# Performance work log

Measured on AMD Instinct MI355X. Metric: run time of the kernel, lower is better.

Reference implementation:

```python
import jax, jax.numpy as jnp
import numpy as np

B, S, H = 2, 1024, 1024
E, I, K = 8, 3584, 2


def setup_inputs() -> dict:
    key = jax.random.key(0)
    k1, k2, k3, k4, k5 = jax.random.split(key, 5)
    scale_h = 1.0 / np.sqrt(H)
    scale_i = 1.0 / np.sqrt(I)
    return {
        "hidden_states": jax.random.normal(k1, (B, S, H), dtype=jnp.float32),
        "gate_w": jax.random.normal(k2, (E, H), dtype=jnp.float32) * scale_h,
        "w1": jax.random.normal(k3, (E, I, H), dtype=jnp.float32) * scale_h,
        "w2": jax.random.normal(k4, (E, H, I), dtype=jnp.float32) * scale_i,
        "w3": jax.random.normal(k5, (E, I, H), dtype=jnp.float32) * scale_h,
    }


def reference(hidden_states, gate_w, w1, w2, w3):
    b, s, h = hidden_states.shape
    x = hidden_states.reshape(-1, h)  # [T, H]
    # router: logits -> float32 softmax -> top-k -> renormalize
    router_logits = x @ gate_w.T  # [T, E]
    probs = jax.nn.softmax(router_logits.astype(jnp.float32), axis=-1)
    topw, topi = jax.lax.top_k(probs, K)  # [T, K]
    topw = topw / jnp.sum(topw, axis=-1, keepdims=True)
    topw = topw.astype(x.dtype)
    # per-token per-expert gate weight (0 for unselected experts) -> dense
    # combine is mathematically identical to gather/scatter dispatch
    gate = jnp.sum(jax.nn.one_hot(topi, E, dtype=x.dtype) * topw[..., None], axis=1)  # [T, E]
    # grouped SwiGLU FFN over all experts
    h1 = jnp.einsum('th,eih->tei', x, w1)
    h3 = jnp.einsum('th,eih->tei', x, w3)
    g = jax.nn.silu(h1) * h3  # [T, E, I]
    y = jnp.einsum('tei,ehi->teh', g, w2)  # [T, E, H]
    out = jnp.einsum('te,teh->th', gate, y)
    return out.reshape(b, s, h)
```

## Files before the change

kernel.cpp:

```cpp
#include <hip/hip_runtime.h>
#include <stdint.h>

#define T_TOK 2048
#define HDIM 1024
#define NEXP 8
#define IDIM 3584
#define MAXTILE 40

#define WS_CNT   0
#define WS_BASE  64
#define WS_TE    128
#define WS_TM    384
#define WS_NT    640
#define WS_TOK   704
#define WS_GW    (WS_TOK + NEXP * T_TOK * 4)
#define WS_XB    (WS_GW + NEXP * T_TOK * 4)
#define WS_G     (WS_XB + T_TOK * HDIM * 2)

typedef __attribute__((ext_vector_type(8))) short bf16x8;
typedef __attribute__((ext_vector_type(16))) float f32x16;

__device__ __forceinline__ unsigned short f2bf(float f) {
    union { float f; unsigned int u; } a; a.f = f;
    unsigned int u = a.u;
    return (unsigned short)((u + 0x7fffu + ((u >> 16) & 1u)) >> 16);
}

__device__ __forceinline__ unsigned int cvt_pk_bf16(float lo, float hi) {
    unsigned int r;
    asm("v_cvt_pk_bf16_f32 %0, %1, %2" : "=v"(r) : "v"(lo), "v"(hi));
    return r;
}

__device__ __forceinline__ uint4 pack8(const float4 a, const float4 b) {
    uint4 r;
    r.x = cvt_pk_bf16(a.x, a.y);
    r.y = cvt_pk_bf16(a.z, a.w);
    r.z = cvt_pk_bf16(b.x, b.y);
    r.w = cvt_pk_bf16(b.z, b.w);
    return r;
}

__device__ __forceinline__ void gload16(const void* gsrc, void* ldst) {
    __builtin_amdgcn_global_load_lds(
        (const __attribute__((address_space(1))) unsigned int*)gsrc,
        (__attribute__((address_space(3))) unsigned int*)ldst, 16, 0, 0);
}

__global__ __launch_bounds__(256) void xcvt_kernel(
    const float* __restrict__ x, unsigned short* __restrict__ xb)
{
    int i = (blockIdx.x * 256 + threadIdx.x) * 8;
    float4 a = *(const float4*)(x + i);
    float4 b = *(const float4*)(x + i + 4);
    *(uint4*)(xb + i) = pack8(a, b);
}

__global__ __launch_bounds__(256) void router_kernel(
    const float* __restrict__ x, const float* __restrict__ gate_w,
    int* __restrict__ cnt, int* __restrict__ tok, float* __restrict__ gw)
{
    int t = blockIdx.x * 4 + (threadIdx.x >> 6);
    int lane = threadIdx.x & 63;
    if (t >= T_TOK) return;
    const float* xr = x + (size_t)t * HDIM;
    float part[NEXP];
#pragma unroll
    for (int e = 0; e < NEXP; e++) part[e] = 0.f;
    for (int h = lane; h < HDIM; h += 64) {
        float xv = xr[h];
#pragma unroll
        for (int e = 0; e < NEXP; e++) part[e] += xv * gate_w[e * HDIM + h];
    }
#pragma unroll
    for (int e = 0; e < NEXP; e++) {
        float v = part[e];
#pragma unroll
        for (int o = 32; o > 0; o >>= 1) v += __shfl_xor(v, o);
        part[e] = v;
    }
    if (lane == 0) {
        int i0 = 0; float v0 = part[0];
#pragma unroll
        for (int e = 1; e < NEXP; e++) if (part[e] > v0) { v0 = part[e]; i0 = e; }
        int i1 = -1; float v1 = -3.4e38f;
#pragma unroll
        for (int e = 0; e < NEXP; e++) if (e != i0 && part[e] > v1) { v1 = part[e]; i1 = e; }
        float d = __expf(v1 - v0);
        float w1v = d / (1.f + d);
        float w0v = 1.f - w1v;
        int p0 = atomicAdd(&cnt[i0], 1);
        tok[i0 * T_TOK + p0] = t; gw[i0 * T_TOK + p0] = w0v;
        int p1 = atomicAdd(&cnt[i1], 1);
        tok[i1 * T_TOK + p1] = t; gw[i1 * T_TOK + p1] = w1v;
    }
}

__global__ void scan_kernel(const int* __restrict__ cnt, int* __restrict__ base,
                            int* __restrict__ tileE, int* __restrict__ tileM,
                            int* __restrict__ ntot)
{
    if (threadIdx.x == 0) {
        int s = 0, nt = 0;
        for (int e = 0; e < NEXP; e++) {
            base[e] = s; s += cnt[e];
            for (int m0 = 0; m0 < cnt[e]; m0 += 128) {
                tileE[nt] = e; tileM[nt] = m0; nt++;
            }
        }
        *ntot = nt;
    }
}

__global__ __launch_bounds__(256, 3) void ffn1_mfma(
    const unsigned short* __restrict__ xb,
    const float* __restrict__ w1,
    const float* __restrict__ w3,
    const int* __restrict__ cnt, const int* __restrict__ base,
    const int* __restrict__ tok,
    const int* __restrict__ tileE, const int* __restrict__ tileM,
    const int* __restrict__ ntot,
    unsigned short* __restrict__ g)
{
    const int ti = blockIdx.y;
    if (ti >= *ntot) return;
    const int e = tileE[ti];
    const int m0 = tileM[ti];
    const int cntE = cnt[e];
    const int i0 = blockIdx.x * 64;
    const int tid = threadIdx.x;
    const int lane = tid & 63;
    const int wid = tid >> 6;

    __shared__ __align__(16) unsigned char lds[49152];

    const int xrr = (lane >> 3);
    const unsigned xoff = ((((unsigned)(lane & 7)) * 16) ^ (((unsigned)xrr) << 4)) >> 1;
    const unsigned short* xsrc[4];
#pragma unroll
    for (int i = 0; i < 4; i++) {
        int row = wid * 32 + i * 8 + xrr;
        int t = tok[e * T_TOK + min(m0 + row, cntE - 1)];
        xsrc[i] = xb + (size_t)t * HDIM + xoff;
    }

    const int rw = tid >> 2;
    const int kq = tid & 3;
    const unsigned swzW = ((unsigned)(rw & 7)) << 4;
    const unsigned wd0 = (((unsigned)kq) * 32) ^ swzW;
    const unsigned wd1 = (((unsigned)kq) * 32 + 16) ^ swzW;
    const float* w1e = w1 + ((size_t)e * IDIM + i0 + rw) * HDIM + kq * 16;
    const float* w3e = w3 + ((size_t)e * IDIM + i0 + rw) * HDIM + kq * 16;

    f32x16 acc1[2], acc3[2];
#pragma unroll
    for (int a = 0; a < 2; a++)
#pragma unroll
        for (int r = 0; r < 16; r++) { acc1[a][r] = 0.f; acc3[a][r] = 0.f; }

    const int wr = wid >> 1;
    const int wc = wid & 1;
    const unsigned lrow = (unsigned)(lane & 31);
    const unsigned lswz = (lrow & 7) << 4;
    const unsigned hi16 = (unsigned)((lane >> 5) * 16);
    const unsigned aRow = (wr * 64 + lrow) * 128;
    const unsigned bRow1 = 32768u + (wc * 32 + lrow) * 128;
    const unsigned bRow3 = 40960u + (wc * 32 + lrow) * 128;

    float4 wva[4], wvb[4];

#pragma unroll
    for (int i = 0; i < 4; i++)
        gload16(xsrc[i], lds + (wid * 32 + i * 8) * 128);
#pragma unroll
    for (int i = 0; i < 4; i++) {
        wva[i] = *(const float4*)(w1e + i * 4);
        wvb[i] = *(const float4*)(w3e + i * 4);
    }

    for (int st = 0; st < HDIM / 64; st++) {
        const unsigned xsb = (unsigned)(st & 1) * 16384u;
        const int k0 = st * 64;
        __syncthreads();
        *(uint4*)(lds + 32768u + rw * 128 + wd0) = pack8(wva[0], wva[1]);
        *(uint4*)(lds + 32768u + rw * 128 + wd1) = pack8(wva[2], wva[3]);
        *(uint4*)(lds + 40960u + rw * 128 + wd0) = pack8(wvb[0], wvb[1]);
        *(uint4*)(lds + 40960u + rw * 128 + wd1) = pack8(wvb[2], wvb[3]);
        __syncthreads();

        if (k0 + 64 < HDIM) {
            const unsigned xnb = xsb ^ 16384u;
#pragma unroll
            for (int i = 0; i < 4; i++)
                gload16(xsrc[i] + k0 + 64, lds + xnb + (wid * 32 + i * 8) * 128);
#pragma unroll
            for (int i = 0; i < 4; i++) {
                wva[i] = *(const float4*)(w1e + k0 + 64 + i * 4);
                wvb[i] = *(const float4*)(w3e + k0 + 64 + i * 4);
            }
        }

#pragma unroll
        for (int s = 0; s < 4; s++) {
            const unsigned off = (((unsigned)(s * 32)) + hi16) ^ lswz;
            bf16x8 a0 = *(const bf16x8*)(lds + xsb + aRow + off);
            bf16x8 a1 = *(const bf16x8*)(lds + xsb + aRow + 32 * 128 + off);
            bf16x8 b1 = *(const bf16x8*)(lds + bRow1 + off);
            bf16x8 b3 = *(const bf16x8*)(lds + bRow3 + off);
            acc1[0] = __builtin_amdgcn_mfma_f32_32x32x16_bf16(a0, b1, acc1[0], 0, 0, 0);
            acc1[1] = __builtin_amdgcn_mfma_f32_32x32x16_bf16(a1, b1, acc1[1], 0, 0, 0);
            acc3[0] = __builtin_amdgcn_mfma_f32_32x32x16_bf16(a0, b3, acc3[0], 0, 0, 0);
            acc3[1] = __builtin_amdgcn_mfma_f32_32x32x16_bf16(a1, b3, acc3[1], 0, 0, 0);
        }
    }

    const int pbase = base[e] + m0;
    const int colI = i0 + wc * 32 + (int)lrow;
    const int rb4 = 4 * (lane >> 5);
#pragma unroll
    for (int ma = 0; ma < 2; ma++) {
#pragma unroll
        for (int r = 0; r < 16; r++) {
            int row = (r & 3) + 8 * (r >> 2) + rb4;
            int m = wr * 64 + ma * 32 + row;
            if (m0 + m < cntE) {
                float h1 = acc1[ma][r], h3 = acc3[ma][r];
                float v = (h1 / (1.f + __expf(-h1))) * h3;
                g[(size_t)(pbase + m) * IDIM + colI] = f2bf(v);
            }
        }
    }
}

__global__ __launch_bounds__(256, 4) void ffn2_mfma(
    const unsigned short* __restrict__ g,
    const float* __restrict__ w2,
    const int* __restrict__ cnt, const int* __restrict__ base,
    const int* __restrict__ tok, const float* __restrict__ gw,
    const int* __restrict__ tileE, const int* __restrict__ tileM,
    const int* __restrict__ ntot,
    float* __restrict__ out)
{
    const int ti = blockIdx.y;
    if (ti >= *ntot) return;
    const int e = tileE[ti];
    const int m0 = tileM[ti];
    const int cntE = cnt[e];
    const int pane = blockIdx.x;
    const int h0 = (pane & 15) * 64;
    const int ks = pane >> 4;
    const int tid = threadIdx.x;
    const int lane = tid & 63;
    const int wid = tid >> 6;

    __shared__ __align__(16) unsigned char lds[40960];

    const int kbeg = ks * (IDIM / 4);

    const int xrr = (lane >> 3);
    const unsigned xoff = ((((unsigned)(lane & 7)) * 16) ^ (((unsigned)xrr) << 4)) >> 1;
    const unsigned short* gsrc[4];
    const int be = base[e];
#pragma unroll
    for (int i = 0; i < 4; i++) {
        int row = wid * 32 + i * 8 + xrr;
        int grow = be + min(m0 + row, cntE - 1);
        gsrc[i] = g + (size_t)grow * IDIM + kbeg + xoff;
    }

    const int rw = tid >> 2;
    const int kq = tid & 3;
    const unsigned swzW = ((unsigned)(rw & 7)) << 4;
    const unsigned wd0 = (((unsigned)kq) * 32) ^ swzW;
    const unsigned wd1 = (((unsigned)kq) * 32 + 16) ^ swzW;
    const float* w2e = w2 + ((size_t)e * HDIM + h0 + rw) * IDIM + kbeg + kq * 16;

    f32x16 acc[2];
#pragma unroll
    for (int a = 0; a < 2; a++)
#pragma unroll
        for (int r = 0; r < 16; r++) acc[a][r] = 0.f;

    const int wr = wid >> 1;
    const int wc = wid & 1;
    const unsigned lrow = (unsigned)(lane & 31);
    const unsigned lswz = (lrow & 7) << 4;
    const unsigned hi16 = (unsigned)((lane >> 5) * 16);
    const unsigned aRow = (wr * 64 + lrow) * 128;
    const unsigned bRow = 32768u + (wc * 32 + lrow) * 128;

    float4 wv[4];
#pragma unroll
    for (int i = 0; i < 4; i++)
        gload16(gsrc[i], lds + (wid * 32 + i * 8) * 128);
#pragma unroll
    for (int i = 0; i < 4; i++)
        wv[i] = *(const float4*)(w2e + i * 4);

    const int NST = (IDIM / 4) / 64;
    for (int st = 0; st < NST; st++) {
        const unsigned xsb = (unsigned)(st & 1) * 16384u;
        const int k0 = st * 64;
        __syncthreads();
        *(uint4*)(lds + 32768u + rw * 128 + wd0) = pack8(wv[0], wv[1]);
        *(uint4*)(lds + 32768u + rw * 128 + wd1) = pack8(wv[2], wv[3]);
        __syncthreads();

        if (st + 1 < NST) {
            const unsigned xnb = xsb ^ 16384u;
#pragma unroll
            for (int i = 0; i < 4; i++)
                gload16(gsrc[i] + k0 + 64, lds + xnb + (wid * 32 + i * 8) * 128);
#pragma unroll
            for (int i = 0; i < 4; i++)
                wv[i] = *(const float4*)(w2e + k0 + 64 + i * 4);
        }

#pragma unroll
        for (int s = 0; s < 4; s++) {
            const unsigned off = (((unsigned)(s * 32)) + hi16) ^ lswz;
            bf16x8 a0 = *(const bf16x8*)(lds + xsb + aRow + off);
            bf16x8 a1 = *(const bf16x8*)(lds + xsb + aRow + 32 * 128 + off);
            bf16x8 b0 = *(const bf16x8*)(lds + bRow + off);
            acc[0] = __builtin_amdgcn_mfma_f32_32x32x16_bf16(a0, b0, acc[0], 0, 0, 0);
            acc[1] = __builtin_amdgcn_mfma_f32_32x32x16_bf16(a1, b0, acc[1], 0, 0, 0);
        }
    }

    const int rb4 = 4 * (lane >> 5);
    const int hcol = h0 + wc * 32 + (int)lrow;
#pragma unroll
    for (int ma = 0; ma < 2; ma++) {
#pragma unroll
        for (int r = 0; r < 16; r++) {
            int row = (r & 3) + 8 * (r >> 2) + rb4;
            int m = wr * 64 + ma * 32 + row;
            if (m0 + m < cntE) {
                int idx = e * T_TOK + m0 + m;
                int t = tok[idx];
                float wgt = gw[idx];
                atomicAdd(out + (size_t)t * HDIM + hcol, wgt * acc[ma][r]);
            }
        }
    }
}

extern "C" void kernel_launch(void* const* d_in, const int* in_sizes, int n_in,
                              void* d_out, int out_size, void* d_ws, size_t ws_size,
                              hipStream_t stream) {
    const float* x      = (const float*)d_in[0];
    const float* gate_w = (const float*)d_in[1];
    const float* w1     = (const float*)d_in[2];
    const float* w2     = (const float*)d_in[3];
    const float* w3     = (const float*)d_in[4];
    float* out = (float*)d_out;
    char* ws = (char*)d_ws;
    int* cnt   = (int*)(ws + WS_CNT);
    int* base  = (int*)(ws + WS_BASE);
    int* tileE = (int*)(ws + WS_TE);
    int* tileM = (int*)(ws + WS_TM);
    int* ntot  = (int*)(ws + WS_NT);
    int* tok   = (int*)(ws + WS_TOK);
    float* gw  = (float*)(ws + WS_GW);
    unsigned short* xb = (unsigned short*)(ws + WS_XB);
    unsigned short* g  = (unsigned short*)(ws + WS_G);

    hipMemsetAsync(cnt, 0, 64, stream);
    hipMemsetAsync(d_out, 0, (size_t)out_size * sizeof(float), stream);

    xcvt_kernel<<<T_TOK * HDIM / (256 * 8), 256, 0, stream>>>(x, xb);
    router_kernel<<<T_TOK / 4, 256, 0, stream>>>(x, gate_w, cnt, tok, gw);
    scan_kernel<<<1, 64, 0, stream>>>(cnt, base, tileE, tileM, ntot);
    ffn1_mfma<<<dim3(IDIM / 64, MAXTILE), 256, 0, stream>>>(xb, w1, w3, cnt, base, tok, tileE, tileM, ntot, g);
    ffn2_mfma<<<dim3(64, MAXTILE), 256, 0, stream>>>(g, w2, cnt, base, tok, gw, tileE, tileM, ntot, out);
}
```

Before: 333.9 us.

## Double-buffer weight tiles in LDS and use a single barrier per k-step

Both FFN kernels now double-buffer the packed bf16 weight tile in LDS alongside the activation tile. Weight registers are prefetched two steps ahead, with explicit vmcnt waits and sched barriers, so each k-iteration needs only one barrier instead of two. The goal is to overlap global weight loads and bf16 packing with MFMA work and to cut synchronisation stalls. In exchange LDS use grows, which lowers the occupancy bounds (ffn1 from 3 to 2 blocks, ffn2 from 4 to 3). The hand-written waitcnt counts must match the exact number of outstanding loads.

```diff
diff --git a/kernel.cpp b/kernel.cpp
--- a/kernel.cpp
+++ b/kernel.cpp
@@ -46,6 +46,8 @@
         (const __attribute__((address_space(1))) unsigned int*)gsrc,
         (__attribute__((address_space(3))) unsigned int*)ldst, 16, 0, 0);
 }
+
+#define SB() __builtin_amdgcn_sched_barrier(0)
 
 __global__ __launch_bounds__(256) void xcvt_kernel(
     const float* __restrict__ x, unsigned short* __restrict__ xb)
@@ -112,7 +114,7 @@
     }
 }
 
-__global__ __launch_bounds__(256, 3) void ffn1_mfma(
+__global__ __launch_bounds__(256, 2) void ffn1_mfma(
     const unsigned short* __restrict__ xb,
     const float* __restrict__ w1,
     const float* __restrict__ w3,
@@ -132,7 +134,7 @@
     const int lane = tid & 63;
     const int wid = tid >> 6;
 
-    __shared__ __align__(16) unsigned char lds[49152];
+    __shared__ __align__(16) unsigned char lds[65536];
 
     const int xrr = (lane >> 3);
     const unsigned xoff = ((((unsigned)(lane & 7)) * 16) ^ (((unsigned)xrr) << 4)) >> 1;
@@ -163,56 +165,71 @@
     const unsigned lrow = (unsigned)(lane & 31);
     const unsigned lswz = (lrow & 7) << 4;
     const unsigned hi16 = (unsigned)((lane >> 5) * 16);
-    const unsigned aRow = (wr * 64 + lrow) * 128;
-    const unsigned bRow1 = 32768u + (wc * 32 + lrow) * 128;
-    const unsigned bRow3 = 40960u + (wc * 32 + lrow) * 128;
+    const unsigned aOff  = (wr * 64 + lrow) * 128;
+    const unsigned b1Off = 16384u + (wc * 32 + lrow) * 128;
+    const unsigned b3Off = 24576u + (wc * 32 + lrow) * 128;
+    const unsigned xdst = (unsigned)(wid * 32) * 128;
 
     float4 wva[4], wvb[4];
 
 #pragma unroll
     for (int i = 0; i < 4; i++)
-        gload16(xsrc[i], lds + (wid * 32 + i * 8) * 128);
+        gload16(xsrc[i], lds + xdst + (unsigned)(i * 8) * 128);
 #pragma unroll
     for (int i = 0; i < 4; i++) {
         wva[i] = *(const float4*)(w1e + i * 4);
         wvb[i] = *(const float4*)(w3e + i * 4);
     }
+    asm volatile("s_waitcnt vmcnt(0)" ::: "memory");
+    *(uint4*)(lds + 16384u + rw * 128 + wd0) = pack8(wva[0], wva[1]);
+    *(uint4*)(lds + 16384u + rw * 128 + wd1) = pack8(wva[2], wva[3]);
+    *(uint4*)(lds + 24576u + rw * 128 + wd0) = pack8(wvb[0], wvb[1]);
+    *(uint4*)(lds + 24576u + rw * 128 + wd1) = pack8(wvb[2], wvb[3]);
+#pragma unroll
+    for (int i = 0; i < 4; i++) {
+        wva[i] = *(const float4*)(w1e + 64 + i * 4);
+        wvb[i] = *(const float4*)(w3e + 64 + i * 4);
+    }
+    __syncthreads();
 
     for (int st = 0; st < HDIM / 64; st++) {
-        const unsigned xsb = (unsigned)(st & 1) * 16384u;
-        const int k0 = st * 64;
-        __syncthreads();
-        *(uint4*)(lds + 32768u + rw * 128 + wd0) = pack8(wva[0], wva[1]);
-        *(uint4*)(lds + 32768u + rw * 128 + wd1) = pack8(wva[2], wva[3]);
-        *(uint4*)(lds + 40960u + rw * 128 + wd0) = pack8(wvb[0], wvb[1]);
-        *(uint4*)(lds + 40960u + rw * 128 + wd1) = pack8(wvb[2], wvb[3]);
-        __syncthreads();
-
-        if (k0 + 64 < HDIM) {
-            const unsigned xnb = xsb ^ 16384u;
-#pragma unroll
-            for (int i = 0; i < 4; i++)
-                gload16(xsrc[i] + k0 + 64, lds + xnb + (wid * 32 + i * 8) * 128);
-#pragma unroll
-            for (int i = 0; i < 4; i++) {
-                wva[i] = *(const float4*)(w1e + k0 + 64 + i * 4);
-                wvb[i] = *(const float4*)(w3e + k0 + 64 + i * 4);
-            }
-        }
-
+        const unsigned cb = (unsigned)(st & 1) * 32768u;
+        const unsigned nb = cb ^ 32768u;
+        SB();
+        const int kg = min((st + 1) * 64, HDIM - 64);
+#pragma unroll
+        for (int i = 0; i < 4; i++)
+            gload16(xsrc[i] + kg, lds + nb + xdst + (unsigned)(i * 8) * 128);
+        SB();
+        *(uint4*)(lds + nb + 16384u + rw * 128 + wd0) = pack8(wva[0], wva[1]);
+        *(uint4*)(lds + nb + 16384u + rw * 128 + wd1) = pack8(wva[2], wva[3]);
+        *(uint4*)(lds + nb + 24576u + rw * 128 + wd0) = pack8(wvb[0], wvb[1]);
+        *(uint4*)(lds + nb + 24576u + rw * 128 + wd1) = pack8(wvb[2], wvb[3]);
+        SB();
+        const int kw = min((st + 2) * 64, HDIM - 64);
+#pragma unroll
+        for (int i = 0; i < 4; i++) {
+            wva[i] = *(const float4*)(w1e + kw + i * 4);
+            wvb[i] = *(const float4*)(w3e + kw + i * 4);
+        }
+        SB();
 #pragma unroll
         for (int s = 0; s < 4; s++) {
             const unsigned off = (((unsigned)(s * 32)) + hi16) ^ lswz;
-            bf16x8 a0 = *(const bf16x8*)(lds + xsb + aRow + off);
-            bf16x8 a1 = *(const bf16x8*)(lds + xsb + aRow + 32 * 128 + off);
-            bf16x8 b1 = *(const bf16x8*)(lds + bRow1 + off);
-            bf16x8 b3 = *(const bf16x8*)(lds + bRow3 + off);
-            acc1[0] = __builtin_amdgcn_mfma_f32_32x32x16_bf16(a0, b1, acc1[0], 0, 0, 0);
-            acc1[1] = __builtin_amdgcn_mfma_f32_32x32x16_bf16(a1, b1, acc1[1], 0, 0, 0);
-            acc3[0] = __builtin_amdgcn_mfma_f32_32x32x16_bf16(a0, b3, acc3[0], 0, 0, 0);
-            acc3[1] = __builtin_amdgcn_mfma_f32_32x32x16_bf16(a1, b3, acc3[1], 0, 0, 0);
-        }
-    }
+            bf16x8 a0 = *(const bf16x8*)(lds + cb + aOff + off);
+            bf16x8 a1 = *(const bf16x8*)(lds + cb + aOff + 32 * 128 + off);
+            bf16x8 p0 = *(const bf16x8*)(lds + cb + b1Off + off);
+            bf16x8 q0 = *(const bf16x8*)(lds + cb + b3Off + off);
+            acc1[0] = __builtin_amdgcn_mfma_f32_32x32x16_bf16(a0, p0, acc1[0], 0, 0, 0);
+            acc1[1] = __builtin_amdgcn_mfma_f32_32x32x16_bf16(a1, p0, acc1[1], 0, 0, 0);
+            acc3[0] = __builtin_amdgcn_mfma_f32_32x32x16_bf16(a0, q0, acc3[0], 0, 0, 0);
+            acc3[1] = __builtin_amdgcn_mfma_f32_32x32x16_bf16(a1, q0, acc3[1], 0, 0, 0);
+        }
+        asm volatile("s_waitcnt vmcnt(8) lgkmcnt(0)" ::: "memory");
+        SB();
+        __builtin_amdgcn_s_barrier();
+    }
+    asm volatile("s_waitcnt vmcnt(0)" ::: "memory");
 
     const int pbase = base[e] + m0;
     const int colI = i0 + wc * 32 + (int)lrow;
@@ -232,7 +249,7 @@
     }
 }
 
-__global__ __launch_bounds__(256, 4) void ffn2_mfma(
+__global__ __launch_bounds__(256, 3) void ffn2_mfma(
     const unsigned short* __restrict__ g,
     const float* __restrict__ w2,
     const int* __restrict__ cnt, const int* __restrict__ base,
@@ -253,9 +270,10 @@
     const int lane = tid & 63;
     const int wid = tid >> 6;
 
-    __shared__ __align__(16) unsigned char lds[40960];
+    __shared__ __align__(16) unsigned char lds[49152];
 
     const int kbeg = ks * (IDIM / 4);
+    const int KSP = IDIM / 4;
 
     const int xrr = (lane >> 3);
     const unsigned xoff = ((((unsigned)(lane & 7)) * 16) ^ (((unsigned)xrr) << 4)) >> 1;
@@ -286,46 +304,58 @@
     const unsigned lrow = (unsigned)(lane & 31);
     const unsigned lswz = (lrow & 7) << 4;
     const unsigned hi16 = (unsigned)((lane >> 5) * 16);
-    const unsigned aRow = (wr * 64 + lrow) * 128;
-    const unsigned bRow = 32768u + (wc * 32 + lrow) * 128;
+    const unsigned aOff = (wr * 64 + lrow) * 128;
+    const unsigned bOff = 16384u + (wc * 32 + lrow) * 128;
+    const unsigned xdst = (unsigned)(wid * 32) * 128;
 
     float4 wv[4];
+
 #pragma unroll
     for (int i = 0; i < 4; i++)
-        gload16(gsrc[i], lds + (wid * 32 + i * 8) * 128);
+        gload16(gsrc[i], lds + xdst + (unsigned)(i * 8) * 128);
 #pragma unroll
     for (int i = 0; i < 4; i++)
         wv[i] = *(const float4*)(w2e + i * 4);
-
-    const int NST = (IDIM / 4) / 64;
+    asm volatile("s_waitcnt vmcnt(0)" ::: "memory");
+    *(uint4*)(lds + 16384u + rw * 128 + wd0) = pack8(wv[0], wv[1]);
+    *(uint4*)(lds + 16384u + rw * 128 + wd1) = pack8(wv[2], wv[3]);
+#pragma unroll
+    for (int i = 0; i < 4; i++)
+        wv[i] = *(const float4*)(w2e + 64 + i * 4);
+    __syncthreads();
+
+    const int NST = KSP / 64;
     for (int st = 0; st < NST; st++) {
-        const unsigned xsb = (unsigned)(st & 1) * 16384u;
-        const int k0 = st * 64;
-        __syncthreads();
-        *(uint4*)(lds + 32768u + rw * 128 + wd0) = pack8(wv[0], wv[1]);
-        *(uint4*)(lds + 32768u + rw * 128 + wd1) = pack8(wv[2], wv[3]);
-        __syncthreads();
-
-        if (st + 1 < NST) {
-            const unsigned xnb = xsb ^ 16384u;
-#pragma unroll
-            for (int i = 0; i < 4; i++)
-                gload16(gsrc[i] + k0 + 64, lds + xnb + (wid * 32 + i * 8) * 128);
-#pragma unroll
-            for (int i = 0; i < 4; i++)
-                wv[i] = *(const float4*)(w2e + k0 + 64 + i * 4);
-        }
-
+        const unsigned cb = (unsigned)(st & 1) * 24576u;
+        const unsigned nb = cb ^ 24576u;
+        SB();
+        const int kg = min((st + 1) * 64, KSP - 64);
+#pragma unroll
+        for (int i = 0; i < 4; i++)
+            gload16(gsrc[i] + kg, lds + nb + xdst + (unsigned)(i * 8) * 128);
+        SB();
+        *(uint4*)(lds + nb + 16384u + rw * 128 + wd0) = pack8(wv[0], wv[1]);
+        *(uint4*)(lds + nb + 16384u + rw * 128 + wd1) = pack8(wv[2], wv[3]);
+        SB();
+        const int kw = min((st + 2) * 64, KSP - 64);
+#pragma unroll
+        for (int i = 0; i < 4; i++)
+            wv[i] = *(const float4*)(w2e + kw + i * 4);
+        SB();
 #pragma unroll
         for (int s = 0; s < 4; s++) {
             const unsigned off = (((unsigned)(s * 32)) + hi16) ^ lswz;
-            bf16x8 a0 = *(const bf16x8*)(lds + xsb + aRow + off);
-            bf16x8 a1 = *(const bf16x8*)(lds + xsb + aRow + 32 * 128 + off);
-            bf16x8 b0 = *(const bf16x8*)(lds + bRow + off);
+            bf16x8 a0 = *(const bf16x8*)(lds + cb + aOff + off);
+            bf16x8 a1 = *(const bf16x8*)(lds + cb + aOff + 32 * 128 + off);
+            bf16x8 b0 = *(const bf16x8*)(lds + cb + bOff + off);
             acc[0] = __builtin_amdgcn_mfma_f32_32x32x16_bf16(a0, b0, acc[0], 0, 0, 0);
             acc[1] = __builtin_amdgcn_mfma_f32_32x32x16_bf16(a1, b0, acc[1], 0, 0, 0);
         }
-    }
+        asm volatile("s_waitcnt vmcnt(4) lgkmcnt(0)" ::: "memory");
+        SB();
+        __builtin_amdgcn_s_barrier();
+    }
+    asm volatile("s_waitcnt vmcnt(0)" ::: "memory");
 
     const int rb4 = 4 * (lane >> 5);
     const int hcol = h0 + wc * 32 + (int)lrow;
```

New measurement: 350.0 us. +4.8%, slower.

## Load activation fragments directly to registers and pipeline weight staging with single barrier

Applied to the files above, without the earlier changes.

Both FFN kernels stop staging the token activations through LDS. Each wave now loads its own 32-row A fragments straight from global memory into registers, and only the bf16-converted weight tiles go through LDS, in a small double buffer with a 32-wide K step. The loop is software-pipelined two and three steps ahead and uses one barrier per step instead of two. Each wave now owns 32 rows across all 64 columns instead of a 64x32 quadrant. LDS use drops sharply, which may help occupancy, but A reads are now uncoalesced per-lane 16-byte global loads and there are twice as many barrier steps.

```diff
diff --git a/kernel.cpp b/kernel.cpp
--- a/kernel.cpp
+++ b/kernel.cpp
@@ -41,12 +41,6 @@
     return r;
 }
 
-__device__ __forceinline__ void gload16(const void* gsrc, void* ldst) {
-    __builtin_amdgcn_global_load_lds(
-        (const __attribute__((address_space(1))) unsigned int*)gsrc,
-        (__attribute__((address_space(3))) unsigned int*)ldst, 16, 0, 0);
-}
-
 __global__ __launch_bounds__(256) void xcvt_kernel(
     const float* __restrict__ x, unsigned short* __restrict__ xb)
 {
@@ -111,6 +105,38 @@
         *ntot = nt;
     }
 }
+
+#define F1_MFMA(AF, RO)                                                        \
+    _Pragma("unroll")                                                          \
+    for (int s = 0; s < 2; s++) {                                              \
+      bf16x8 b1a = *(const bf16x8*)(lds + (RO) + bfo[0][s]);                   \
+      bf16x8 b1b = *(const bf16x8*)(lds + (RO) + bfo[1][s]);                   \
+      bf16x8 b3a = *(const bf16x8*)(lds + 8192u + (RO) + bfo[0][s]);           \
+      bf16x8 b3b = *(const bf16x8*)(lds + 8192u + (RO) + bfo[1][s]);           \
+      acc1[0] = __builtin_amdgcn_mfma_f32_32x32x16_bf16(AF[s], b1a, acc1[0], 0, 0, 0); \
+      acc1[1] = __builtin_amdgcn_mfma_f32_32x32x16_bf16(AF[s], b1b, acc1[1], 0, 0, 0); \
+      acc3[0] = __builtin_amdgcn_mfma_f32_32x32x16_bf16(AF[s], b3a, acc3[0], 0, 0, 0); \
+      acc3[1] = __builtin_amdgcn_mfma_f32_32x32x16_bf16(AF[s], b3b, acc3[1], 0, 0, 0); \
+    }
+
+#define F1_STEP(ST, AF, W1C, W3C)                                              \
+  {                                                                            \
+    F1_MFMA(AF, ((unsigned)((ST) & 1)) * 4096u)                                \
+    const unsigned wo = ((unsigned)(((ST) + 1) & 1)) * 4096u;                  \
+    *(uint4*)(lds + wo + wdst) = pack8(W1C[0], W1C[1]);                        \
+    *(uint4*)(lds + 8192u + wo + wdst) = pack8(W3C[0], W3C[1]);                \
+    const int ka = min(((ST) + 2) * 32, HDIM - 32);                            \
+    AF[0] = *(const bf16x8*)(arow + ka);                                       \
+    AF[1] = *(const bf16x8*)(arow + ka + 16);                                  \
+    const int kw = min(((ST) + 3) * 32, HDIM - 32);                            \
+    W1C[0] = *(const float4*)(w1e + kw);                                       \
+    W1C[1] = *(const float4*)(w1e + kw + 4);                                   \
+    W3C[0] = *(const float4*)(w3e + kw);                                       \
+    W3C[1] = *(const float4*)(w3e + kw + 4);                                   \
+    asm volatile("s_waitcnt lgkmcnt(0)" ::: "memory");                         \
+    __builtin_amdgcn_sched_barrier(0);                                         \
+    __builtin_amdgcn_s_barrier();                                              \
+  }
 
 __global__ __launch_bounds__(256, 3) void ffn1_mfma(
     const unsigned short* __restrict__ xb,
@@ -132,25 +158,34 @@
     const int lane = tid & 63;
     const int wid = tid >> 6;
 
-    __shared__ __align__(16) unsigned char lds[49152];
-
-    const int xrr = (lane >> 3);
-    const unsigned xoff = ((((unsigned)(lane & 7)) * 16) ^ (((unsigned)xrr) << 4)) >> 1;
-    const unsigned short* xsrc[4];
-#pragma unroll
-    for (int i = 0; i < 4; i++) {
-        int row = wid * 32 + i * 8 + xrr;
+    __shared__ __align__(16) unsigned char lds[16384];
+
+    const int fr = lane & 31;
+    const int hi = lane >> 5;
+
+    const unsigned short* arow;
+    {
+        int row = wid * 32 + fr;
         int t = tok[e * T_TOK + min(m0 + row, cntE - 1)];
-        xsrc[i] = xb + (size_t)t * HDIM + xoff;
-    }
-
-    const int rw = tid >> 2;
-    const int kq = tid & 3;
-    const unsigned swzW = ((unsigned)(rw & 7)) << 4;
-    const unsigned wd0 = (((unsigned)kq) * 32) ^ swzW;
-    const unsigned wd1 = (((unsigned)kq) * 32 + 16) ^ swzW;
-    const float* w1e = w1 + ((size_t)e * IDIM + i0 + rw) * HDIM + kq * 16;
-    const float* w3e = w3 + ((size_t)e * IDIM + i0 + rw) * HDIM + kq * 16;
+        arow = xb + (size_t)t * HDIM + hi * 8;
+    }
+
+    unsigned bfo[2][2];
+#pragma unroll
+    for (int f2 = 0; f2 < 2; f2++)
+#pragma unroll
+        for (int s = 0; s < 2; s++) {
+            unsigned row = (unsigned)(f2 * 32 + fr);
+            unsigned slot = ((unsigned)(s * 2 + hi)) ^ ((row >> 1) & 3u);
+            bfo[f2][s] = row * 64u + slot * 16u;
+        }
+
+    const int srow = tid >> 2;
+    const int c4 = tid & 3;
+    const unsigned wdst = (unsigned)srow * 64u +
+                          (((unsigned)c4 ^ (((unsigned)srow >> 1) & 3u)) * 16u);
+    const float* w1e = w1 + ((size_t)e * IDIM + i0 + srow) * HDIM + c4 * 8;
+    const float* w3e = w3 + ((size_t)e * IDIM + i0 + srow) * HDIM + c4 * 8;
 
     f32x16 acc1[2], acc3[2];
 #pragma unroll
@@ -158,79 +193,74 @@
 #pragma unroll
         for (int r = 0; r < 16; r++) { acc1[a][r] = 0.f; acc3[a][r] = 0.f; }
 
-    const int wr = wid >> 1;
-    const int wc = wid & 1;
-    const unsigned lrow = (unsigned)(lane & 31);
-    const unsigned lswz = (lrow & 7) << 4;
-    const unsigned hi16 = (unsigned)((lane >> 5) * 16);
-    const unsigned aRow = (wr * 64 + lrow) * 128;
-    const unsigned bRow1 = 32768u + (wc * 32 + lrow) * 128;
-    const unsigned bRow3 = 40960u + (wc * 32 + lrow) * 128;
-
-    float4 wva[4], wvb[4];
-
-#pragma unroll
-    for (int i = 0; i < 4; i++)
-        gload16(xsrc[i], lds + (wid * 32 + i * 8) * 128);
-#pragma unroll
-    for (int i = 0; i < 4; i++) {
-        wva[i] = *(const float4*)(w1e + i * 4);
-        wvb[i] = *(const float4*)(w3e + i * 4);
-    }
-
-    for (int st = 0; st < HDIM / 64; st++) {
-        const unsigned xsb = (unsigned)(st & 1) * 16384u;
-        const int k0 = st * 64;
-        __syncthreads();
-        *(uint4*)(lds + 32768u + rw * 128 + wd0) = pack8(wva[0], wva[1]);
-        *(uint4*)(lds + 32768u + rw * 128 + wd1) = pack8(wva[2], wva[3]);
-        *(uint4*)(lds + 40960u + rw * 128 + wd0) = pack8(wvb[0], wvb[1]);
-        *(uint4*)(lds + 40960u + rw * 128 + wd1) = pack8(wvb[2], wvb[3]);
-        __syncthreads();
-
-        if (k0 + 64 < HDIM) {
-            const unsigned xnb = xsb ^ 16384u;
-#pragma unroll
-            for (int i = 0; i < 4; i++)
-                gload16(xsrc[i] + k0 + 64, lds + xnb + (wid * 32 + i * 8) * 128);
-#pragma unroll
-            for (int i = 0; i < 4; i++) {
-                wva[i] = *(const float4*)(w1e + k0 + 64 + i * 4);
-                wvb[i] = *(const float4*)(w3e + k0 + 64 + i * 4);
-            }
-        }
-
-#pragma unroll
-        for (int s = 0; s < 4; s++) {
-            const unsigned off = (((unsigned)(s * 32)) + hi16) ^ lswz;
-            bf16x8 a0 = *(const bf16x8*)(lds + xsb + aRow + off);
-            bf16x8 a1 = *(const bf16x8*)(lds + xsb + aRow + 32 * 128 + off);
-            bf16x8 b1 = *(const bf16x8*)(lds + bRow1 + off);
-            bf16x8 b3 = *(const bf16x8*)(lds + bRow3 + off);
-            acc1[0] = __builtin_amdgcn_mfma_f32_32x32x16_bf16(a0, b1, acc1[0], 0, 0, 0);
-            acc1[1] = __builtin_amdgcn_mfma_f32_32x32x16_bf16(a1, b1, acc1[1], 0, 0, 0);
-            acc3[0] = __builtin_amdgcn_mfma_f32_32x32x16_bf16(a0, b3, acc3[0], 0, 0, 0);
-            acc3[1] = __builtin_amdgcn_mfma_f32_32x32x16_bf16(a1, b3, acc3[1], 0, 0, 0);
-        }
+    bf16x8 af0[2], af1[2];
+    float4 w1cA[2], w3cA[2], w1cB[2], w3cB[2];
+
+    {
+        float4 t0 = *(const float4*)(w1e);
+        float4 t1 = *(const float4*)(w1e + 4);
+        float4 t2 = *(const float4*)(w3e);
+        float4 t3 = *(const float4*)(w3e + 4);
+        *(uint4*)(lds + wdst) = pack8(t0, t1);
+        *(uint4*)(lds + 8192u + wdst) = pack8(t2, t3);
+    }
+    af0[0] = *(const bf16x8*)(arow);
+    af0[1] = *(const bf16x8*)(arow + 16);
+    af1[0] = *(const bf16x8*)(arow + 32);
+    af1[1] = *(const bf16x8*)(arow + 48);
+    w1cA[0] = *(const float4*)(w1e + 32);  w1cA[1] = *(const float4*)(w1e + 36);
+    w3cA[0] = *(const float4*)(w3e + 32);  w3cA[1] = *(const float4*)(w3e + 36);
+    w1cB[0] = *(const float4*)(w1e + 64);  w1cB[1] = *(const float4*)(w1e + 68);
+    w3cB[0] = *(const float4*)(w3e + 64);  w3cB[1] = *(const float4*)(w3e + 68);
+    asm volatile("s_waitcnt lgkmcnt(0)" ::: "memory");
+    __builtin_amdgcn_sched_barrier(0);
+    __builtin_amdgcn_s_barrier();
+
+#pragma unroll 1
+    for (int dd = 0; dd < HDIM / 64; dd++) {
+        F1_STEP(2 * dd,     af0, w1cA, w3cA);
+        F1_STEP(2 * dd + 1, af1, w1cB, w3cB);
     }
 
     const int pbase = base[e] + m0;
-    const int colI = i0 + wc * 32 + (int)lrow;
-    const int rb4 = 4 * (lane >> 5);
-#pragma unroll
-    for (int ma = 0; ma < 2; ma++) {
+    const int rb4 = 4 * hi;
+#pragma unroll
+    for (int f2 = 0; f2 < 2; f2++) {
 #pragma unroll
         for (int r = 0; r < 16; r++) {
             int row = (r & 3) + 8 * (r >> 2) + rb4;
-            int m = wr * 64 + ma * 32 + row;
+            int m = wid * 32 + row;
             if (m0 + m < cntE) {
-                float h1 = acc1[ma][r], h3 = acc3[ma][r];
+                float h1 = acc1[f2][r], h3 = acc3[f2][r];
                 float v = (h1 / (1.f + __expf(-h1))) * h3;
-                g[(size_t)(pbase + m) * IDIM + colI] = f2bf(v);
+                g[(size_t)(pbase + m) * IDIM + i0 + f2 * 32 + fr] = f2bf(v);
             }
         }
     }
 }
+
+#define F2_STEP(ST, AF, W2C)                                                   \
+  {                                                                            \
+    const unsigned ro = ((unsigned)((ST) & 1)) * 4096u;                        \
+    _Pragma("unroll")                                                          \
+    for (int s = 0; s < 2; s++) {                                              \
+      bf16x8 b0 = *(const bf16x8*)(lds + ro + bfo[0][s]);                      \
+      bf16x8 b1 = *(const bf16x8*)(lds + ro + bfo[1][s]);                      \
+      acc[0] = __builtin_amdgcn_mfma_f32_32x32x16_bf16(AF[s], b0, acc[0], 0, 0, 0); \
+      acc[1] = __builtin_amdgcn_mfma_f32_32x32x16_bf16(AF[s], b1, acc[1], 0, 0, 0); \
+    }                                                                          \
+    const unsigned wo = ((unsigned)(((ST) + 1) & 1)) * 4096u;                  \
+    *(uint4*)(lds + wo + wdst) = pack8(W2C[0], W2C[1]);                        \
+    const int ka = min(((ST) + 2) * 32, KSP - 32);                             \
+    AF[0] = *(const bf16x8*)(grow_p + ka);                                     \
+    AF[1] = *(const bf16x8*)(grow_p + ka + 16);                                \
+    const int kw = min(((ST) + 3) * 32, KSP - 32);                             \
+    W2C[0] = *(const float4*)(w2e + kw);                                       \
+    W2C[1] = *(const float4*)(w2e + kw + 4);                                   \
+    asm volatile("s_waitcnt lgkmcnt(0)" ::: "memory");                         \
+    __builtin_amdgcn_sched_barrier(0);                                         \
+    __builtin_amdgcn_s_barrier();                                              \
+  }
 
 __global__ __launch_bounds__(256, 4) void ffn2_mfma(
     const unsigned short* __restrict__ g,
@@ -253,27 +283,36 @@
     const int lane = tid & 63;
     const int wid = tid >> 6;
 
-    __shared__ __align__(16) unsigned char lds[40960];
-
-    const int kbeg = ks * (IDIM / 4);
-
-    const int xrr = (lane >> 3);
-    const unsigned xoff = ((((unsigned)(lane & 7)) * 16) ^ (((unsigned)xrr) << 4)) >> 1;
-    const unsigned short* gsrc[4];
-    const int be = base[e];
-#pragma unroll
-    for (int i = 0; i < 4; i++) {
-        int row = wid * 32 + i * 8 + xrr;
-        int grow = be + min(m0 + row, cntE - 1);
-        gsrc[i] = g + (size_t)grow * IDIM + kbeg + xoff;
-    }
-
-    const int rw = tid >> 2;
-    const int kq = tid & 3;
-    const unsigned swzW = ((unsigned)(rw & 7)) << 4;
-    const unsigned wd0 = (((unsigned)kq) * 32) ^ swzW;
-    const unsigned wd1 = (((unsigned)kq) * 32 + 16) ^ swzW;
-    const float* w2e = w2 + ((size_t)e * HDIM + h0 + rw) * IDIM + kbeg + kq * 16;
+    __shared__ __align__(16) unsigned char lds[8192];
+
+    const int KSP = IDIM / 4;
+    const int kbeg = ks * KSP;
+
+    const int fr = lane & 31;
+    const int hi = lane >> 5;
+
+    const unsigned short* grow_p;
+    {
+        int row = wid * 32 + fr;
+        int gr = base[e] + min(m0 + row, cntE - 1);
+        grow_p = g + (size_t)gr * IDIM + kbeg + hi * 8;
+    }
+
+    unsigned bfo[2][2];
+#pragma unroll
+    for (int f2 = 0; f2 < 2; f2++)
+#pragma unroll
+        for (int s = 0; s < 2; s++) {
+            unsigned row = (unsigned)(f2 * 32 + fr);
+            unsigned slot = ((unsigned)(s * 2 + hi)) ^ ((row >> 1) & 3u);
+            bfo[f2][s] = row * 64u + slot * 16u;
+        }
+
+    const int srow = tid >> 2;
+    const int c4 = tid & 3;
+    const unsigned wdst = (unsigned)srow * 64u +
+                          (((unsigned)c4 ^ (((unsigned)srow >> 1) & 3u)) * 16u);
+    const float* w2e = w2 + ((size_t)e * HDIM + h0 + srow) * IDIM + kbeg + c4 * 8;
 
     f32x16 acc[2];
 #pragma unroll
@@ -281,65 +320,43 @@
 #pragma unroll
         for (int r = 0; r < 16; r++) acc[a][r] = 0.f;
 
-    const int wr = wid >> 1;
-    const int wc = wid & 1;
-    const unsigned lrow = (unsigned)(lane & 31);
-    const unsigned lswz = (lrow & 7) << 4;
-    const unsigned hi16 = (unsigned)((lane >> 5) * 16);
-    const unsigned aRow = (wr * 64 + lrow) * 128;
-    const unsigned bRow = 32768u + (wc * 32 + lrow) * 128;
-
-    float4 wv[4];
-#pragma unroll
-    for (int i = 0; i < 4; i++)
-        gload16(gsrc[i], lds + (wid * 32 + i * 8) * 128);
-#pragma unroll
-    for (int i = 0; i < 4; i++)
-        wv[i] = *(const float4*)(w2e + i * 4);
-
-    const int NST = (IDIM / 4) / 64;
-    for (int st = 0; st < NST; st++) {
-        const unsigned xsb = (unsigned)(st & 1) * 16384u;
-        const int k0 = st * 64;
-        __syncthreads();
-        *(uint4*)(lds + 32768u + rw * 128 + wd0) = pack8(wv[0], wv[1]);
-        *(uint4*)(lds + 32768u + rw * 128 + wd1) = pack8(wv[2], wv[3]);
-        __syncthreads();
-
-        if (st + 1 < NST) {
-            const unsigned xnb = xsb ^ 16384u;
-#pragma unroll
-            for (int i = 0; i < 4; i++)
-                gload16(gsrc[i] + k0 + 64, lds + xnb + (wid * 32 + i * 8) * 128);
-#pragma unroll
-            for (int i = 0; i < 4; i++)
-                wv[i] = *(const float4*)(w2e + k0 + 64 + i * 4);
-        }
-
-#pragma unroll
-        for (int s = 0; s < 4; s++) {
-            const unsigned off = (((unsigned)(s * 32)) + hi16) ^ lswz;
-            bf16x8 a0 = *(const bf16x8*)(lds + xsb + aRow + off);
-            bf16x8 a1 = *(const bf16x8*)(lds + xsb + aRow + 32 * 128 + off);
-            bf16x8 b0 = *(const bf16x8*)(lds + bRow + off);
-            acc[0] = __builtin_amdgcn_mfma_f32_32x32x16_bf16(a0, b0, acc[0], 0, 0, 0);
-            acc[1] = __builtin_amdgcn_mfma_f32_32x32x16_bf16(a1, b0, acc[1], 0, 0, 0);
-        }
-    }
-
-    const int rb4 = 4 * (lane >> 5);
-    const int hcol = h0 + wc * 32 + (int)lrow;
-#pragma unroll
-    for (int ma = 0; ma < 2; ma++) {
+    bf16x8 af0[2], af1[2];
+    float4 w2cA[2], w2cB[2];
+
+    {
+        float4 t0 = *(const float4*)(w2e);
+        float4 t1 = *(const float4*)(w2e + 4);
+        *(uint4*)(lds + wdst) = pack8(t0, t1);
+    }
+    af0[0] = *(const bf16x8*)(grow_p);
+    af0[1] = *(const bf16x8*)(grow_p + 16);
+    af1[0] = *(const bf16x8*)(grow_p + 32);
+    af1[1] = *(const bf16x8*)(grow_p + 48);
+    w2cA[0] = *(const float4*)(w2e + 32);  w2cA[1] = *(const float4*)(w2e + 36);
+    w2cB[0] = *(const float4*)(w2e + 64);  w2cB[1] = *(const float4*)(w2e + 68);
+    asm volatile("s_waitcnt lgkmcnt(0)" ::: "memory");
+    __builtin_amdgcn_sched_barrier(0);
+    __builtin_amdgcn_s_barrier();
+
+#pragma unroll 1
+    for (int dd = 0; dd < (IDIM / 4) / 64; dd++) {
+        F2_STEP(2 * dd,     af0, w2cA);
+        F2_STEP(2 * dd + 1, af1, w2cB);
+    }
+
+    const int rb4 = 4 * hi;
+#pragma unroll
+    for (int f2 = 0; f2 < 2; f2++) {
 #pragma unroll
         for (int r = 0; r < 16; r++) {
             int row = (r & 3) + 8 * (r >> 2) + rb4;
-            int m = wr * 64 + ma * 32 + row;
+            int m = wid * 32 + row;
             if (m0 + m < cntE) {
                 int idx = e * T_TOK + m0 + m;
                 int t = tok[idx];
                 float wgt = gw[idx];
-                atomicAdd(out + (size_t)t * HDIM + hcol, wgt * acc[ma][r]);
+                atomicAdd(out + (size_t)t * HDIM + h0 + f2 * 32 + fr,
+                          wgt * acc[f2][r]);
             }
         }
     }
```

After: 367.8 us. +10.1%, slower.

## Enlarge ffn1 token tile to 256 rows with separate tile lists per FFN

Applied to the files above, without the earlier changes.

The scan now builds two tile lists: 256-token tiles for the first FFN and 128-token tiles for the second. ffn1 is restructured so each wave computes 64 rows by 64 columns with a 2x2 MFMA grid per weight, using a K step of 32 and a new chunked LDS layout without swizzling. The aim is to halve how often each w1/w3 tile is re-read and converted per expert, roughly doubling reuse of the fp32 weight stream. In exchange it uses more accumulator registers (occupancy bound drops to 2), doubles the number of K iterations and barriers, and may introduce LDS bank conflicts.

```diff
diff --git a/kernel.cpp b/kernel.cpp
--- a/kernel.cpp
+++ b/kernel.cpp
@@ -5,13 +5,17 @@
 #define HDIM 1024
 #define NEXP 8
 #define IDIM 3584
-#define MAXTILE 40
+#define MAXT1 24
+#define MAXT2 40
 
 #define WS_CNT   0
 #define WS_BASE  64
-#define WS_TE    128
-#define WS_TM    384
-#define WS_NT    640
+#define WS_TE1   128
+#define WS_TM1   224
+#define WS_TE2   320
+#define WS_TM2   480
+#define WS_NT1   640
+#define WS_NT2   644
 #define WS_TOK   704
 #define WS_GW    (WS_TOK + NEXP * T_TOK * 4)
 #define WS_XB    (WS_GW + NEXP * T_TOK * 4)
@@ -97,22 +101,23 @@
 }
 
 __global__ void scan_kernel(const int* __restrict__ cnt, int* __restrict__ base,
-                            int* __restrict__ tileE, int* __restrict__ tileM,
-                            int* __restrict__ ntot)
+                            int* __restrict__ tE1, int* __restrict__ tM1,
+                            int* __restrict__ nt1p,
+                            int* __restrict__ tE2, int* __restrict__ tM2,
+                            int* __restrict__ nt2p)
 {
     if (threadIdx.x == 0) {
-        int s = 0, nt = 0;
+        int s = 0, n1 = 0, n2 = 0;
         for (int e = 0; e < NEXP; e++) {
             base[e] = s; s += cnt[e];
-            for (int m0 = 0; m0 < cnt[e]; m0 += 128) {
-                tileE[nt] = e; tileM[nt] = m0; nt++;
-            }
-        }
-        *ntot = nt;
-    }
-}
-
-__global__ __launch_bounds__(256, 3) void ffn1_mfma(
+            for (int m0 = 0; m0 < cnt[e]; m0 += 256) { tE1[n1] = e; tM1[n1] = m0; n1++; }
+            for (int m0 = 0; m0 < cnt[e]; m0 += 128) { tE2[n2] = e; tM2[n2] = m0; n2++; }
+        }
+        *nt1p = n1; *nt2p = n2;
+    }
+}
+
+__global__ __launch_bounds__(256, 2) void ffn1_mfma(
     const unsigned short* __restrict__ xb,
     const float* __restrict__ w1,
     const float* __restrict__ w3,
@@ -132,101 +137,99 @@
     const int lane = tid & 63;
     const int wid = tid >> 6;
 
-    __shared__ __align__(16) unsigned char lds[49152];
-
-    const int xrr = (lane >> 3);
-    const unsigned xoff = ((((unsigned)(lane & 7)) * 16) ^ (((unsigned)xrr) << 4)) >> 1;
+    __shared__ __align__(16) unsigned char lds[40960];
+
     const unsigned short* xsrc[4];
-#pragma unroll
-    for (int i = 0; i < 4; i++) {
-        int row = wid * 32 + i * 8 + xrr;
+    {
+        int row = wid * 64 + lane;
         int t = tok[e * T_TOK + min(m0 + row, cntE - 1)];
-        xsrc[i] = xb + (size_t)t * HDIM + xoff;
-    }
-
-    const int rw = tid >> 2;
+#pragma unroll
+        for (int q = 0; q < 4; q++)
+            xsrc[q] = xb + (size_t)t * HDIM + q * 8;
+    }
+    const unsigned xldst = (unsigned)(wid * 1024);
+
+    const int srow = tid >> 2;
     const int kq = tid & 3;
-    const unsigned swzW = ((unsigned)(rw & 7)) << 4;
-    const unsigned wd0 = (((unsigned)kq) * 32) ^ swzW;
-    const unsigned wd1 = (((unsigned)kq) * 32 + 16) ^ swzW;
-    const float* w1e = w1 + ((size_t)e * IDIM + i0 + rw) * HDIM + kq * 16;
-    const float* w3e = w3 + ((size_t)e * IDIM + i0 + rw) * HDIM + kq * 16;
-
-    f32x16 acc1[2], acc3[2];
+    const unsigned wdst = (unsigned)(kq * 1024 + srow * 16);
+    const float* w1e = w1 + ((size_t)e * IDIM + i0 + srow) * HDIM + kq * 8;
+    const float* w3e = w3 + ((size_t)e * IDIM + i0 + srow) * HDIM + kq * 8;
+
+    f32x16 acc1[2][2], acc3[2][2];
 #pragma unroll
     for (int a = 0; a < 2; a++)
 #pragma unroll
-        for (int r = 0; r < 16; r++) { acc1[a][r] = 0.f; acc3[a][r] = 0.f; }
-
-    const int wr = wid >> 1;
-    const int wc = wid & 1;
-    const unsigned lrow = (unsigned)(lane & 31);
-    const unsigned lswz = (lrow & 7) << 4;
-    const unsigned hi16 = (unsigned)((lane >> 5) * 16);
-    const unsigned aRow = (wr * 64 + lrow) * 128;
-    const unsigned bRow1 = 32768u + (wc * 32 + lrow) * 128;
-    const unsigned bRow3 = 40960u + (wc * 32 + lrow) * 128;
-
-    float4 wva[4], wvb[4];
-
-#pragma unroll
-    for (int i = 0; i < 4; i++)
-        gload16(xsrc[i], lds + (wid * 32 + i * 8) * 128);
-#pragma unroll
-    for (int i = 0; i < 4; i++) {
-        wva[i] = *(const float4*)(w1e + i * 4);
-        wvb[i] = *(const float4*)(w3e + i * 4);
-    }
-
-    for (int st = 0; st < HDIM / 64; st++) {
+        for (int b = 0; b < 2; b++)
+#pragma unroll
+            for (int r = 0; r < 16; r++) { acc1[a][b][r] = 0.f; acc3[a][b][r] = 0.f; }
+
+    const int fr = lane & 31;
+    const int hi = lane >> 5;
+
+    float4 wva[2], wvb[2];
+
+#pragma unroll
+    for (int q = 0; q < 4; q++)
+        gload16(xsrc[q], lds + (unsigned)(q * 4096) + xldst);
+    wva[0] = *(const float4*)(w1e);  wva[1] = *(const float4*)(w1e + 4);
+    wvb[0] = *(const float4*)(w3e);  wvb[1] = *(const float4*)(w3e + 4);
+
+    const int NST = HDIM / 32;
+#pragma unroll 1
+    for (int st = 0; st < NST; st++) {
         const unsigned xsb = (unsigned)(st & 1) * 16384u;
-        const int k0 = st * 64;
         __syncthreads();
-        *(uint4*)(lds + 32768u + rw * 128 + wd0) = pack8(wva[0], wva[1]);
-        *(uint4*)(lds + 32768u + rw * 128 + wd1) = pack8(wva[2], wva[3]);
-        *(uint4*)(lds + 40960u + rw * 128 + wd0) = pack8(wvb[0], wvb[1]);
-        *(uint4*)(lds + 40960u + rw * 128 + wd1) = pack8(wvb[2], wvb[3]);
+        *(uint4*)(lds + 32768u + wdst) = pack8(wva[0], wva[1]);
+        *(uint4*)(lds + 36864u + wdst) = pack8(wvb[0], wvb[1]);
         __syncthreads();
 
-        if (k0 + 64 < HDIM) {
+        if (st + 1 < NST) {
+            const int kn = (st + 1) * 32;
             const unsigned xnb = xsb ^ 16384u;
 #pragma unroll
-            for (int i = 0; i < 4; i++)
-                gload16(xsrc[i] + k0 + 64, lds + xnb + (wid * 32 + i * 8) * 128);
-#pragma unroll
-            for (int i = 0; i < 4; i++) {
-                wva[i] = *(const float4*)(w1e + k0 + 64 + i * 4);
-                wvb[i] = *(const float4*)(w3e + k0 + 64 + i * 4);
-            }
-        }
-
-#pragma unroll
-        for (int s = 0; s < 4; s++) {
-            const unsigned off = (((unsigned)(s * 32)) + hi16) ^ lswz;
-            bf16x8 a0 = *(const bf16x8*)(lds + xsb + aRow + off);
-            bf16x8 a1 = *(const bf16x8*)(lds + xsb + aRow + 32 * 128 + off);
-            bf16x8 b1 = *(const bf16x8*)(lds + bRow1 + off);
-            bf16x8 b3 = *(const bf16x8*)(lds + bRow3 + off);
-            acc1[0] = __builtin_amdgcn_mfma_f32_32x32x16_bf16(a0, b1, acc1[0], 0, 0, 0);
-            acc1[1] = __builtin_amdgcn_mfma_f32_32x32x16_bf16(a1, b1, acc1[1], 0, 0, 0);
-            acc3[0] = __builtin_amdgcn_mfma_f32_32x32x16_bf16(a0, b3, acc3[0], 0, 0, 0);
-            acc3[1] = __builtin_amdgcn_mfma_f32_32x32x16_bf16(a1, b3, acc3[1], 0, 0, 0);
+            for (int q = 0; q < 4; q++)
+                gload16(xsrc[q] + kn, lds + xnb + (unsigned)(q * 4096) + xldst);
+            wva[0] = *(const float4*)(w1e + kn);  wva[1] = *(const float4*)(w1e + kn + 4);
+            wvb[0] = *(const float4*)(w3e + kn);  wvb[1] = *(const float4*)(w3e + kn + 4);
+        }
+
+#pragma unroll
+        for (int c = 0; c < 2; c++) {
+            const unsigned ch = (unsigned)((c * 2 + hi) * 4096);
+            const unsigned chw = (unsigned)((c * 2 + hi) * 1024);
+            bf16x8 a0 = *(const bf16x8*)(lds + xsb + ch + (wid * 64 + fr) * 16);
+            bf16x8 a1 = *(const bf16x8*)(lds + xsb + ch + (wid * 64 + 32 + fr) * 16);
+            bf16x8 p0 = *(const bf16x8*)(lds + 32768u + chw + fr * 16);
+            bf16x8 p1 = *(const bf16x8*)(lds + 32768u + chw + (32 + fr) * 16);
+            bf16x8 q0 = *(const bf16x8*)(lds + 36864u + chw + fr * 16);
+            bf16x8 q1 = *(const bf16x8*)(lds + 36864u + chw + (32 + fr) * 16);
+            acc1[0][0] = __builtin_amdgcn_mfma_f32_32x32x16_bf16(a0, p0, acc1[0][0], 0, 0, 0);
+            acc1[0][1] = __builtin_amdgcn_mfma_f32_32x32x16_bf16(a0, p1, acc1[0][1], 0, 0, 0);
+            acc1[1][0] = __builtin_amdgcn_mfma_f32_32x32x16_bf16(a1, p0, acc1[1][0], 0, 0, 0);
+            acc1[1][1] = __builtin_amdgcn_mfma_f32_32x32x16_bf16(a1, p1, acc1[1][1], 0, 0, 0);
+            acc3[0][0] = __builtin_amdgcn_mfma_f32_32x32x16_bf16(a0, q0, acc3[0][0], 0, 0, 0);
+            acc3[0][1] = __builtin_amdgcn_mfma_f32_32x32x16_bf16(a0, q1, acc3[0][1], 0, 0, 0);
+            acc3[1][0] = __builtin_amdgcn_mfma_f32_32x32x16_bf16(a1, q0, acc3[1][0], 0, 0, 0);
+            acc3[1][1] = __builtin_amdgcn_mfma_f32_32x32x16_bf16(a1, q1, acc3[1][1], 0, 0, 0);
         }
     }
 
     const int pbase = base[e] + m0;
-    const int colI = i0 + wc * 32 + (int)lrow;
-    const int rb4 = 4 * (lane >> 5);
-#pragma unroll
-    for (int ma = 0; ma < 2; ma++) {
+    const int rb4 = 4 * hi;
+#pragma unroll
+    for (int m = 0; m < 2; m++) {
 #pragma unroll
         for (int r = 0; r < 16; r++) {
             int row = (r & 3) + 8 * (r >> 2) + rb4;
-            int m = wr * 64 + ma * 32 + row;
-            if (m0 + m < cntE) {
-                float h1 = acc1[ma][r], h3 = acc3[ma][r];
-                float v = (h1 / (1.f + __expf(-h1))) * h3;
-                g[(size_t)(pbase + m) * IDIM + colI] = f2bf(v);
+            int mm = wid * 64 + m * 32 + row;
+            if (m0 + mm < cntE) {
+                unsigned short* grow = g + (size_t)(pbase + mm) * IDIM + i0 + fr;
+#pragma unroll
+                for (int n = 0; n < 2; n++) {
+                    float h1 = acc1[m][n][r], h3 = acc3[m][n][r];
+                    float v = (h1 / (1.f + __expf(-h1))) * h3;
+                    grow[n * 32] = f2bf(v);
+                }
             }
         }
     }
@@ -357,9 +360,12 @@
     char* ws = (char*)d_ws;
     int* cnt   = (int*)(ws + WS_CNT);
     int* base  = (int*)(ws + WS_BASE);
-    int* tileE = (int*)(ws + WS_TE);
-    int* tileM = (int*)(ws + WS_TM);
-    int* ntot  = (int*)(ws + WS_NT);
+    int* tE1   = (int*)(ws + WS_TE1);
+    int* tM1   = (int*)(ws + WS_TM1);
+    int* tE2   = (int*)(ws + WS_TE2);
+    int* tM2   = (int*)(ws + WS_TM2);
+    int* nt1   = (int*)(ws + WS_NT1);
+    int* nt2   = (int*)(ws + WS_NT2);
     int* tok   = (int*)(ws + WS_TOK);
     float* gw  = (float*)(ws + WS_GW);
     unsigned short* xb = (unsigned short*)(ws + WS_XB);
@@ -370,7 +376,7 @@
 
     xcvt_kernel<<<T_TOK * HDIM / (256 * 8), 256, 0, stream>>>(x, xb);
     router_kernel<<<T_TOK / 4, 256, 0, stream>>>(x, gate_w, cnt, tok, gw);
-    scan_kernel<<<1, 64, 0, stream>>>(cnt, base, tileE, tileM, ntot);
-    ffn1_mfma<<<dim3(IDIM / 64, MAXTILE), 256, 0, stream>>>(xb, w1, w3, cnt, base, tok, tileE, tileM, ntot, g);
-    ffn2_mfma<<<dim3(64, MAXTILE), 256, 0, stream>>>(g, w2, cnt, base, tok, gw, tileE, tileM, ntot, out);
-}
+    scan_kernel<<<1, 64, 0, stream>>>(cnt, base, tE1, tM1, nt1, tE2, tM2, nt2);
+    ffn1_mfma<<<dim3(IDIM / 64, MAXT1), 256, 0, stream>>>(xb, w1, w3, cnt, base, tok, tE1, tM1, nt1, g);
+    ffn2_mfma<<<dim3(64, MAXT2), 256, 0, stream>>>(g, w2, cnt, base, tok, gw, tE2, tM2, nt2, out);
+}
```

After: 379.7 us. +13.7%, slower.
